# Kernel tuning notes

Hardware: AMD Instinct MI355X
Metric: run time of the kernel (lower is better)

The kernel has to match this reference:

```python
import jax, jax.numpy as jnp
import numpy as np

N, E, D, EDGE_DIM = 50000, 150000, 100, 200

def _w(key, fi, fo):
    return jax.random.normal(key, (fi, fo), dtype=jnp.float32) / np.float32(np.sqrt(fi))

def setup_inputs():
    key = jax.random.key(0)
    ks = jax.random.split(key, 40)
    inp = {}
    inp["x"] = jax.random.normal(ks[0], (N, D), dtype=jnp.float32)
    inp["msg"] = jax.random.normal(ks[1], (E, D), dtype=jnp.float32)
    # TimeEncoder: Linear(1, D)
    inp["time_w"] = _w(ks[2], 1, D)
    inp["time_b"] = jnp.zeros((D,), jnp.float32)
    # TransformerConv 1: in=100, heads=8, out=100, concat -> 800
    H1 = 8 * D
    inp["c1_qw"] = _w(ks[3], D, H1); inp["c1_qb"] = jnp.zeros((H1,), jnp.float32)
    inp["c1_kw"] = _w(ks[4], D, H1); inp["c1_kb"] = jnp.zeros((H1,), jnp.float32)
    inp["c1_vw"] = _w(ks[5], D, H1); inp["c1_vb"] = jnp.zeros((H1,), jnp.float32)
    inp["c1_ew"] = _w(ks[6], EDGE_DIM, H1)  # lin_edge has no bias in PyG
    inp["c1_sw"] = _w(ks[7], D, H1); inp["c1_sb"] = jnp.zeros((H1,), jnp.float32)
    # TransformerConv 2: in=800, heads=1, out=100, concat=False
    inp["c2_qw"] = _w(ks[8], H1, D); inp["c2_qb"] = jnp.zeros((D,), jnp.float32)
    inp["c2_kw"] = _w(ks[9], H1, D); inp["c2_kb"] = jnp.zeros((D,), jnp.float32)
    inp["c2_vw"] = _w(ks[10], H1, D); inp["c2_vb"] = jnp.zeros((D,), jnp.float32)
    inp["c2_ew"] = _w(ks[11], EDGE_DIM, D)
    inp["c2_sw"] = _w(ks[12], H1, D); inp["c2_sb"] = jnp.zeros((D,), jnp.float32)
    # LinkPredictor (in_channels=100, out=2)
    inp["lp_src_w"] = _w(ks[13], D, 2 * D); inp["lp_src_b"] = jnp.zeros((2 * D,), jnp.float32)
    inp["lp_dst_w"] = _w(ks[14], D, 2 * D); inp["lp_dst_b"] = jnp.zeros((2 * D,), jnp.float32)
    inp["lp1_w"] = _w(ks[15], 4 * D, 8 * D); inp["lp1_b"] = jnp.zeros((8 * D,), jnp.float32)
    inp["lp2_w"] = _w(ks[16], 8 * D, 2 * D); inp["lp2_b"] = jnp.zeros((2 * D,), jnp.float32)
    inp["lp3_w"] = _w(ks[17], 2 * D, D // 2); inp["lp3_b"] = jnp.zeros((D // 2,), jnp.float32)
    inp["lp4_w"] = _w(ks[18], D // 2, 2); inp["lp4_b"] = jnp.zeros((2,), jnp.float32)
    inp["last_update"] = jax.random.randint(ks[19], (N,), 0, 1000000)
    inp["t"] = jax.random.randint(ks[20], (E,), 0, 1000000)
    inp["edge_index"] = jax.random.randint(ks[21], (2, E), 0, N)
    return inp

def _tconv(x, src, dst, edge_attr, qw, qb, kw, kb, vw, vb, ew, sw, sb, heads, out_ch, concat, n):
    q = (x @ qw + qb).reshape(n, heads, out_ch)
    k = (x @ kw + kb).reshape(n, heads, out_ch)
    v = (x @ vw + vb).reshape(n, heads, out_ch)
    e = (edge_attr @ ew).reshape(-1, heads, out_ch)        # [E,H,C]
    kj = k[src] + e                                        # gather src keys + edge
    alpha = jnp.sum(q[dst] * kj, axis=-1) / np.float32(np.sqrt(out_ch))  # [E,H]
    amax = jax.ops.segment_max(alpha, dst, num_segments=n)
    ex = jnp.exp(alpha - amax[dst])
    denom = jax.ops.segment_sum(ex, dst, num_segments=n)
    a = ex / (denom[dst] + 1e-16)                          # per-dest softmax
    agg = jax.ops.segment_sum((v[src] + e) * a[..., None], dst, num_segments=n)
    out = agg.reshape(n, heads * out_ch) if concat else jnp.mean(agg, axis=1)
    return out + x @ sw + sb                               # root/skip connection

def reference(x, msg, time_w, time_b,
              c1_qw, c1_qb, c1_kw, c1_kb, c1_vw, c1_vb, c1_ew, c1_sw, c1_sb,
              c2_qw, c2_qb, c2_kw, c2_kb, c2_vw, c2_vb, c2_ew, c2_sw, c2_sb,
              lp_src_w, lp_src_b, lp_dst_w, lp_dst_b,
              lp1_w, lp1_b, lp2_w, lp2_b, lp3_w, lp3_b, lp4_w, lp4_b,
              last_update, t, edge_index):
    src, dst = edge_index[0], edge_index[1]
    rel_t = (last_update[src] - t).astype(jnp.float32)[:, None]  # [E,1]
    rel_enc = jnp.cos(rel_t @ time_w + time_b)                   # [E,D]
    edge_attr = jnp.concatenate([rel_enc, msg], axis=-1)         # [E,200]
    h = jax.nn.relu(_tconv(x, src, dst, edge_attr, c1_qw, c1_qb, c1_kw, c1_kb,
                           c1_vw, c1_vb, c1_ew, c1_sw, c1_sb, 8, D, True, N))
    h = jax.nn.relu(_tconv(h, src, dst, edge_attr, c2_qw, c2_qb, c2_kw, c2_kb,
                           c2_vw, c2_vb, c2_ew, c2_sw, c2_sb, 1, D, False, N))
    hh = jnp.concatenate([h[src] @ lp_src_w + lp_src_b,
                          h[dst] @ lp_dst_w + lp_dst_b], axis=-1)
    hh = jnp.tanh(hh @ lp1_w + lp1_b)
    hh = jnp.tanh(hh @ lp2_w + lp2_b)
    hh = jnp.tanh(hh @ lp3_w + lp3_b)
    return hh @ lp4_w + lp4_b
```

## Files before the change

kernel.cpp:

```cpp
#include <hip/hip_runtime.h>
#include <hip/hip_bf16.h>
#include <math.h>

typedef __hip_bfloat16 bf16;
typedef short s16x8 __attribute__((ext_vector_type(8)));
typedef float f32x4 __attribute__((ext_vector_type(4)));

#define NN 50000
#define EE 150000
#define EH 75000

static __device__ __forceinline__ float b2f(bf16 x){ return __bfloat162float(x); }
static __device__ __forceinline__ bf16 f2b(float x){ return __float2bfloat16(x); }
static __device__ __forceinline__ short f2s(float x){
  union { bf16 b; short s; } u; u.b = f2b(x); return u.s;
}
static __device__ __forceinline__ float u2f_lo(unsigned u){ union{unsigned i;float f;}c; c.i=u<<16; return c.f; }
static __device__ __forceinline__ float u2f_hi(unsigned u){ union{unsigned i;float f;}c; c.i=u&0xffff0000u; return c.f; }

static __device__ __forceinline__ float fast_tanh(float x){
  float a = fabsf(x);
  float e = __expf(2.0f*a);
  float t = 1.0f - __fdividef(2.0f, e + 1.0f);
  return x < 0.f ? -t : t;
}

static __device__ __forceinline__ void gload_lds16(const void* g, void* l){
  __builtin_amdgcn_global_load_lds((const __attribute__((address_space(1))) void*)g,
                                   (__attribute__((address_space(3))) void*)l, 16, 0, 0);
}

template<int N> static __device__ __forceinline__ void wait_vmcnt(){
  if constexpr(N==0) asm volatile("s_waitcnt vmcnt(0)" ::: "memory");
  else if constexpr(N==1) asm volatile("s_waitcnt vmcnt(1)" ::: "memory");
  else if constexpr(N==2) asm volatile("s_waitcnt vmcnt(2)" ::: "memory");
  else if constexpr(N==3) asm volatile("s_waitcnt vmcnt(3)" ::: "memory");
  else if constexpr(N==4) asm volatile("s_waitcnt vmcnt(4)" ::: "memory");
  else if constexpr(N==5) asm volatile("s_waitcnt vmcnt(5)" ::: "memory");
  else asm volatile("s_waitcnt vmcnt(6)" ::: "memory");
}
static __device__ __forceinline__ void wait_lgkm0(){
  asm volatile("s_waitcnt lgkmcnt(0)" ::: "memory");
}
static __device__ __forceinline__ void memfence(){
  asm volatile("" ::: "memory");
}

__global__ void k_zero(int* __restrict__ p, int n){
  int i = blockIdx.x*blockDim.x + threadIdx.x;
  if(i<n) p[i]=0;
}

__global__ void k_hist(const int* __restrict__ dst, int* __restrict__ deg){
  int i = blockIdx.x*blockDim.x + threadIdx.x;
  if(i<EE) atomicAdd(&deg[dst[i]], 1);
}

__global__ void k_scan(const int* __restrict__ deg, int* __restrict__ rowptr){
  __shared__ int part[1024];
  int tid = threadIdx.x;
  const int n = NN;
  int chunk = (n + 1023)/1024;
  int start = tid*chunk;
  int end = start + chunk; if(end > n) end = n;
  int s = 0;
  for(int i=start;i<end;i++) s += deg[i];
  part[tid] = s; __syncthreads();
  for(int off=1; off<1024; off<<=1){
    int v = (tid>=off)? part[tid-off] : 0;
    __syncthreads();
    part[tid] += v;
    __syncthreads();
  }
  int run = (tid==0)? 0 : part[tid-1];
  for(int i=start;i<end;i++){ rowptr[i]=run; run += deg[i]; }
  if(tid==0) rowptr[n] = part[1023];
}

__global__ void k_scatter(const int* __restrict__ dst, const int* __restrict__ srcv,
                          const int* __restrict__ rowptr,
                          int* __restrict__ cursor, int* __restrict__ elist,
                          int* __restrict__ ssrc){
  int e = blockIdx.x*blockDim.x + threadIdx.x;
  if(e<EE){
    int d=dst[e]; int p=atomicAdd(&cursor[d],1);
    int pos = rowptr[d]+p;
    elist[pos]=e; ssrc[pos]=srcv[e];
  }
}

__global__ void k_relenc(const int* __restrict__ elist, const int* __restrict__ ssrc,
                         const int* __restrict__ tt, const int* __restrict__ lu,
                         const float* __restrict__ tw, const float* __restrict__ tb,
                         bf16* __restrict__ rel){
  int i = blockIdx.x*blockDim.x + threadIdx.x;
  if(i >= EE*112) return;
  int j = i/112, c = i - j*112;
  float v = 0.f;
  if(c < 100){
    int e = elist[j];
    float rt  = (float)(lu[ssrc[j]] - tt[e]);
    float arg = __fadd_rn(__fmul_rn(rt, tw[c]), tb[c]);
    v = cosf(arg);
  }
  rel[i] = f2b(v);
}

__global__ void k_cvtpad(const float* __restrict__ in, int incols,
                         bf16* __restrict__ outp, int outcols, int total){
  int i = blockIdx.x*blockDim.x + threadIdx.x;
  if(i >= total) return;
  int r = i/outcols, c = i - r*outcols;
  outp[i] = f2b(c < incols ? in[(size_t)r*incols + c] : 0.f);
}

__global__ void k_wt2(const float* __restrict__ W, int K, int N, int colofs, int ncols,
                      bf16* __restrict__ WT, int kpad, int nrows){
  int i = blockIdx.x*blockDim.x + threadIdx.x;
  if(i >= nrows*kpad) return;
  int n = i / kpad, k = i - n*kpad;
  float v = (n<ncols && k<K)? W[(size_t)k*N + colofs + n] : 0.f;
  WT[i] = f2b(v);
}

__global__ void k_wtc1(const float* __restrict__ qw, const float* __restrict__ kw,
                       const float* __restrict__ vw, bf16* __restrict__ outp){
  int i = blockIdx.x*blockDim.x + threadIdx.x;
  if(i >= 8*320*128) return;
  int h = i/(320*128), r = (i/128)%320, k = i&127;
  float v = 0.f;
  if(r < 300 && k < 100){
    int s = r/100, n = r - s*100;
    const float* W = s==0? qw : s==1? kw : vw;
    v = W[(size_t)k*800 + h*100 + n];
  }
  outp[i] = f2b(v);
}

__global__ void k_wte(const float* __restrict__ ew, int N, int colofs,
                      bf16* __restrict__ outp){
  int i = blockIdx.x*blockDim.x + threadIdx.x;
  if(i >= 112*256) return;
  int r = i>>8, k = i&255;
  float v = 0.f;
  if(r < 100){
    if(k < 100) v = ew[(size_t)k*N + colofs + r];
    else if(k >= 128 && k < 228) v = ew[(size_t)(k-28)*N + colofs + r];
  }
  outp[i] = f2b(v);
}

__global__ void k_bstack3(const float* __restrict__ b0, const float* __restrict__ b1,
                          const float* __restrict__ b2, int W, int H,
                          float* __restrict__ outp){
  int i = blockIdx.x*blockDim.x + threadIdx.x;
  if(i >= H*3*W) return;
  int h = i/(3*W), r = i - h*3*W, s = r/W, c = r - s*W;
  const float* b = s==0? b0 : s==1? b1 : b2;
  outp[i] = b[h*W + c];
}

__global__ void k_foldw(const float* __restrict__ sw, const float* __restrict__ dw,
                        const float* __restrict__ w1, bf16* __restrict__ o){
  int i = blockIdx.x*blockDim.x + threadIdx.x;
  if(i >= 800*224) return;
  int n = i/224, k = i - n*224;
  float s = 0.f;
  if(k < 100){
    for(int j=0;j<200;j++) s += sw[k*200+j]*w1[(size_t)j*800+n];
  } else if(k >= 112 && k < 212){
    int kk = k-112;
    for(int j=0;j<200;j++) s += dw[kk*200+j]*w1[(size_t)(200+j)*800+n];
  }
  o[i] = f2b(s);
}
__global__ void k_foldb(const float* __restrict__ sb, const float* __restrict__ db,
                        const float* __restrict__ w1, const float* __restrict__ b1,
                        float* __restrict__ o){
  int n = blockIdx.x*blockDim.x + threadIdx.x;
  if(n >= 800) return;
  float s = b1[n];
  for(int j=0;j<200;j++) s += sb[j]*w1[(size_t)j*800+n] + db[j]*w1[(size_t)(200+j)*800+n];
  o[n] = s;
}

template<int NT>
static __device__ void mm_body(
    char* lds, int bx, int nstrip,
    const bf16* __restrict__ A1, int lda1, int kv1, const int* __restrict__ g1,
    int KS,
    const bf16* __restrict__ A2b, int lda2b, int kv2b, const int* __restrict__ g2,
    const float* __restrict__ A2f, int lda2f, int kv2f,
    const bf16* __restrict__ WT, int kpad,
    const bf16* __restrict__ zbuf,
    const float* __restrict__ bias,
    bf16* __restrict__ C, int ldc,
    int M, int nvalid, int act)
{
  constexpr int BN = NT*16;
  constexpr int BPASS = (BN*4 + 255)/256;
  constexpr int ABYTES = 8192;
  constexpr int BUFSZ = ABYTES + BPASS*4096;

  const int tid  = threadIdx.x;
  const int wave = tid>>6, lane = tid&63;
  const int quad = lane>>4, lo = lane&15;
  WT += (size_t)nstrip*BN*kpad;
  C  += (size_t)nstrip*BN;
  if(bias) bias += nstrip*BN;
  const int nval = nvalid - nstrip*BN;
  const int row0 = bx*128;

  float bvr[NT];
#pragma unroll
  for(int n=0;n<NT;n++){
    int col = n*16 + lo;
    bvr[n] = (bias && col < nval) ? bias[col] : 0.f;
  }
#pragma unroll
  for(int n=0;n<NT;n++) asm volatile("" :: "v"(bvr[n]));

  const char*  a1b[2];
  const char*  a2bp[2];
  const float* f2base[2];
  int acol0[2];
#pragma unroll
  for(int p=0;p<2;p++){
    int s = p*256 + tid;
    int row = s>>2, cp = s&3;
    int q = cp ^ ((row>>1)&3);
    int col0 = q*8;
    int rg = row0 + row; if(rg > M-1) rg = M-1;
    int r1 = g1 ? g1[rg] : rg;
    int r2 = g2 ? g2[rg] : rg;
    acol0[p] = col0;
    a1b[p]   = (const char*)A1 + ((size_t)r1*lda1 + col0)*2;
    a2bp[p]  = A2b ? (const char*)A2b + ((size_t)r2*lda2b)*2 : nullptr;
    f2base[p]= A2f ? (A2f + (size_t)r2*lda2f) : nullptr;
  }
  const char* bbase[BPASS];
#pragma unroll
  for(int p=0;p<BPASS;p++){
    int s = p*256 + tid;
    int rb = s>>2; if(rb > BN-1) rb = BN-1;
    int cp = s&3;
    int lq = cp ^ ((rb>>1)&3);
    bbase[p] = (const char*)WT + ((size_t)rb*kpad + lq*8)*2;
  }

  f32x4 acc[2][NT];
#pragma unroll
  for(int m=0;m<2;m++)
#pragma unroll
    for(int n=0;n<NT;n++) acc[m][n] = (f32x4){0.f,0.f,0.f,0.f};

  float4 pf0[2], pf1[2];

  auto stageA1 = [&](char* buf, int kb){
#pragma unroll
    for(int p=0;p<2;p++){
      int k = kb + acol0[p];
      const char* s;
      if(k < KS) s = (k < kv1) ? (a1b[p] + (size_t)kb*2) : (const char*)zbuf;
      else { int o = k - KS; s = (o < kv2b) ? (a2bp[p] + (size_t)o*2) : (const char*)zbuf; }
      gload_lds16(s, buf + p*4096 + wave*1024);
    }
  };
  auto loadA2f = [&](int kb){
#pragma unroll
    for(int p=0;p<2;p++){
      int o = kb + acol0[p] - KS;
      const float* ap = f2base[p] + o;
      pf0[p] = (o   < kv2f) ? *(const float4*)ap     : (float4){0.f,0.f,0.f,0.f};
      pf1[p] = (o+4 < kv2f) ? *(const float4*)(ap+4) : (float4){0.f,0.f,0.f,0.f};
    }
  };
  auto writeA2 = [&](char* buf){
#pragma unroll
    for(int p=0;p<2;p++){
      s16x8 v;
      v[0]=f2s(pf0[p].x); v[1]=f2s(pf0[p].y); v[2]=f2s(pf0[p].z); v[3]=f2s(pf0[p].w);
      v[4]=f2s(pf1[p].x); v[5]=f2s(pf1[p].y); v[6]=f2s(pf1[p].z); v[7]=f2s(pf1[p].w);
      *(s16x8*)(buf + p*4096 + (size_t)tid*16) = v;
    }
  };
  auto stageB = [&](char* buf, int kb){
#pragma unroll
    for(int p=0;p<BPASS;p++)
      gload_lds16(bbase[p] + (size_t)kb*2, buf + ABYTES + p*4096 + wave*1024);
  };
  auto compute = [&](const char* buf){
    s16x8 af[2];
#pragma unroll
    for(int m=0;m<2;m++){
      int rl = wave*32 + m*16 + lo;
      int cp = quad ^ ((rl>>1)&3);
      af[m] = *(const s16x8*)(buf + rl*64 + cp*16);
    }
#pragma unroll
    for(int n=0;n<NT;n++){
      int rb = n*16 + lo;
      int cp = quad ^ ((rb>>1)&3);
      s16x8 bfr = *(const s16x8*)(buf + ABYTES + rb*64 + cp*16);
      acc[0][n] = __builtin_amdgcn_mfma_f32_16x16x32_bf16(af[0], bfr, acc[0][n], 0,0,0);
      acc[1][n] = __builtin_amdgcn_mfma_f32_16x16x32_bf16(af[1], bfr, acc[1][n], 0,0,0);
    }
  };

  const int T = kpad >> 5;
  stageA1(lds, 0); stageB(lds, 0);
  if(T > 1){ stageA1(lds + BUFSZ, 32); stageB(lds + BUFSZ, 32); }

  for(int t=0; t<T; t++){
    bool nb  = (t+1 < T);
    bool nfp = nb && A2f && (((t+1)<<5) >= KS);
    if(!nb)      wait_vmcnt<0>();
    else if(nfp) wait_vmcnt<BPASS>();
    else         wait_vmcnt<2+BPASS>();
    wait_lgkm0();
    __builtin_amdgcn_s_barrier();
    memfence();
    int tp = t+2;
    bool sp  = (tp < T);
    bool spf = sp && A2f && ((tp<<5) >= KS);
    char* nb3 = lds + (tp%3)*BUFSZ;
    if(sp){
      int kb2 = tp<<5;
      if(spf) loadA2f(kb2);
      else    stageA1(nb3, kb2);
      stageB(nb3, kb2);
    }
    compute(lds + (t%3)*BUFSZ);
    if(spf) writeA2(nb3);
  }

  const int r0 = (lane&1)<<1;
#pragma unroll
  for(int n=0;n<NT;n++){
    int col  = n*16 + lo;
    int pcol = col & ~1;
    bool cok = (pcol < nval);
    float bv = bvr[n];
#pragma unroll
    for(int m=0;m<2;m++){
      float v[4];
#pragma unroll
      for(int r=0;r<4;r++){
        float t = acc[m][n][r] + bv;
        if(act==1) t = fmaxf(t, 0.f);
        else if(act==2) t = fast_tanh(t);
        v[r] = t;
      }
      unsigned mylo = (unsigned)(unsigned short)f2s(v[r0])
                    | ((unsigned)(unsigned short)f2s(v[r0+1])<<16);
      unsigned snd  = (unsigned)(unsigned short)f2s(v[r0^2])
                    | ((unsigned)(unsigned short)f2s(v[(r0^2)+1])<<16);
      unsigned got  = (unsigned)__shfl_xor((int)snd, 1);
      unsigned w0, w1;
      if(lane&1){ w0 = (got & 0xffffu) | (mylo<<16); w1 = (got>>16) | (mylo & 0xffff0000u); }
      else      { w0 = (mylo & 0xffffu) | (got<<16); w1 = (mylo>>16) | (got & 0xffff0000u); }
      if(cok){
        int prow = row0 + wave*32 + m*16 + quad*4 + r0;
        if(prow   < M) *(unsigned*)(C + (size_t)prow*ldc + pcol) = w0;
        if(prow+1 < M) *(unsigned*)(C + (size_t)(prow+1)*ldc + pcol) = w1;
      }
    }
  }
}

template<int NT>
__global__ __launch_bounds__(256) void mm_tile(
    const bf16* A1, int lda1, int kv1, const int* g1, int KS,
    const bf16* A2b, int lda2b, int kv2b, const int* g2,
    const float* A2f, int lda2f, int kv2f,
    const bf16* WT, int kpad, const bf16* zbuf, const float* bias,
    bf16* C, int ldc, int M, int nvalid, int act)
{
  constexpr int BUFSZ = 8192 + ((NT*16*4+255)/256)*4096;
  __shared__ __align__(16) char lds[3*BUFSZ];
  mm_body<NT>(lds, blockIdx.x, blockIdx.y, A1,lda1,kv1,g1, KS,
              A2b,lda2b,kv2b,g2, A2f,lda2f,kv2f, WT,kpad, zbuf, bias,
              C,ldc, M,nvalid,act);
}

template<int NT>
__global__ __launch_bounds__(256) void mm_gath(
    const bf16* __restrict__ A, int lda, int KS,
    const int* __restrict__ gs, const int* __restrict__ gd,
    const bf16* __restrict__ WT,
    const float* __restrict__ bias,
    bf16* __restrict__ C, int ldc,
    int M, int nvalid, int act)
{
  constexpr int T = 7;
  constexpr int KPAD = 224;
  constexpr int BN = NT*16;
  constexpr int BPASS = (BN*4 + 255)/256;
  constexpr int BUFSZ = BPASS*4096;
  __shared__ __align__(16) char lds[3*BUFSZ];

  const int tid  = threadIdx.x;
  const int wave = tid>>6, lane = tid&63;
  const int quad = lane>>4, lo = lane&15;
  const int nstrip = blockIdx.y;
  const bf16* WTs = WT + (size_t)nstrip*BN*KPAD;
  C += (size_t)nstrip*BN;
  const float* bp = bias ? bias + nstrip*BN : nullptr;
  const int nval = nvalid - nstrip*BN;
  const int row0 = blockIdx.x*128;

  float bvr[NT];
#pragma unroll
  for(int n=0;n<NT;n++){
    int col = n*16 + lo;
    bvr[n] = (bp && col < nval) ? bp[col] : 0.f;
  }

  const bf16* abase[2][2];
#pragma unroll
  for(int m=0;m<2;m++){
    int r = row0 + wave*32 + m*16 + lo; if(r > M-1) r = M-1;
    abase[m][0] = A + (size_t)gs[r]*lda;
    abase[m][1] = A + (size_t)gd[r]*lda;
  }

  s16x8 areg[T][2];
#pragma unroll
  for(int t=0;t<T;t++){
#pragma unroll
    for(int m=0;m<2;m++){
      int k = t*32 + quad*8;
      const bf16* p = (k < KS) ? (abase[m][0] + k) : (abase[m][1] + (k - KS));
      asm volatile("global_load_dwordx4 %0, %1, off"
                   : "=v"(areg[t][m]) : "v"(p));
    }
  }
  memfence();

  const char* bbase[BPASS];
#pragma unroll
  for(int p=0;p<BPASS;p++){
    int s = p*256 + tid;
    int rb = s>>2; if(rb > BN-1) rb = BN-1;
    int cp = s&3;
    int lq = cp ^ ((rb>>1)&3);
    bbase[p] = (const char*)WTs + ((size_t)rb*KPAD + lq*8)*2;
  }
  auto stageB = [&](char* buf, int kb){
#pragma unroll
    for(int p=0;p<BPASS;p++)
      gload_lds16(bbase[p] + (size_t)kb*2, buf + p*4096 + wave*1024);
  };

  f32x4 acc[2][NT];
#pragma unroll
  for(int m=0;m<2;m++)
#pragma unroll
    for(int n=0;n<NT;n++) acc[m][n] = (f32x4){0.f,0.f,0.f,0.f};

  stageB(lds, 0);
  stageB(lds + BUFSZ, 32);

#pragma unroll
  for(int t=0; t<T; t++){
    if(t < T-1) wait_vmcnt<BPASS>();
    else        wait_vmcnt<0>();
    wait_lgkm0();
    __builtin_amdgcn_s_barrier();
    memfence();
    if(t+2 < T) stageB(lds + ((t+2)%3)*BUFSZ, (t+2)*32);
    const char* buf = lds + (t%3)*BUFSZ;
#pragma unroll
    for(int n=0;n<NT;n++){
      int rb = n*16 + lo;
      int cp = quad ^ ((rb>>1)&3);
      s16x8 bfr = *(const s16x8*)(buf + rb*64 + cp*16);
      acc[0][n] = __builtin_amdgcn_mfma_f32_16x16x32_bf16(areg[t][0], bfr, acc[0][n], 0,0,0);
      acc[1][n] = __builtin_amdgcn_mfma_f32_16x16x32_bf16(areg[t][1], bfr, acc[1][n], 0,0,0);
    }
  }

  const int r0 = (lane&1)<<1;
#pragma unroll
  for(int n=0;n<NT;n++){
    int col  = n*16 + lo;
    int pcol = col & ~1;
    bool cok = (pcol < nval);
    float bv = bvr[n];
#pragma unroll
    for(int m=0;m<2;m++){
      float v[4];
#pragma unroll
      for(int r=0;r<4;r++){
        float t = acc[m][n][r] + bv;
        if(act==1) t = fmaxf(t, 0.f);
        else if(act==2) t = fast_tanh(t);
        v[r] = t;
      }
      unsigned mylo = (unsigned)(unsigned short)f2s(v[r0])
                    | ((unsigned)(unsigned short)f2s(v[r0+1])<<16);
      unsigned snd  = (unsigned)(unsigned short)f2s(v[r0^2])
                    | ((unsigned)(unsigned short)f2s(v[(r0^2)+1])<<16);
      unsigned got  = (unsigned)__shfl_xor((int)snd, 1);
      unsigned w0, w1;
      if(lane&1){ w0 = (got & 0xffffu) | (mylo<<16); w1 = (got>>16) | (mylo & 0xffff0000u); }
      else      { w0 = (mylo & 0xffffu) | (got<<16); w1 = (mylo>>16) | (got & 0xffff0000u); }
      if(cok){
        int prow = row0 + wave*32 + m*16 + quad*4 + r0;
        if(prow   < M) *(unsigned*)(C + (size_t)prow*ldc + pcol) = w0;
        if(prow+1 < M) *(unsigned*)(C + (size_t)(prow+1)*ldc + pcol) = w1;
      }
    }
  }
}

__global__ __launch_bounds__(256) void k_attn(
    const int* __restrict__ rowptr, const int* __restrict__ ssrc,
    const bf16* __restrict__ qkv, const bf16* __restrict__ ehc,
    bf16* __restrict__ hout, int ldh, int colofs, int zpad)
{
  int wave = threadIdx.x>>6, lane = threadIdx.x&63;
  int node = blockIdx.x*4 + wave;
  if(node >= NN) return;
  bool act = (lane < 50);
  float q0=0.f, q1=0.f;
  const unsigned* qrow = (const unsigned*)(qkv + (size_t)node*300);
  if(act){ unsigned u = qrow[lane]; q0=u2f_lo(u); q1=u2f_hi(u); }
  int s0 = rowptr[node], s1 = rowptr[node+1];
  float m = -3.4e38f, d = 0.f, a0 = 0.f, a1 = 0.f;
  for(int j=s0; j<s1; j++){
    int sn = ssrc[j];
    float p = 0.f, e0=0.f, e1=0.f;
    if(act){
      unsigned uk = ((const unsigned*)(qkv + (size_t)sn*300 + 100))[lane];
      unsigned ue = ((const unsigned*)(ehc + (size_t)j*100))[lane];
      e0=u2f_lo(ue); e1=u2f_hi(ue);
      p = q0*(u2f_lo(uk)+e0) + q1*(u2f_hi(uk)+e1);
    }
    for(int off=32; off; off>>=1) p += __shfl_xor(p, off);
    float alpha = p * 0.1f;
    float mn = fmaxf(m, alpha);
    float sc = __expf(m - mn);
    float wv = __expf(alpha - mn);
    d = d*sc + wv;
    if(act){
      unsigned uv = ((const unsigned*)(qkv + (size_t)sn*300 + 200))[lane];
      a0 = a0*sc + wv*(u2f_lo(uv)+e0);
      a1 = a1*sc + wv*(u2f_hi(uv)+e1);
    }
    m = mn;
  }
  if(act){
    float inv = 1.f/(d + 1e-16f);
    unsigned us = ((const unsigned*)(hout + (size_t)node*ldh + colofs))[lane];
    float h0 = fmaxf(u2f_lo(us) + a0*inv, 0.f);
    float h1 = fmaxf(u2f_hi(us) + a1*inv, 0.f);
    bf16* op = hout + (size_t)node*ldh + colofs + lane*2;
    op[0] = f2b(h0); op[1] = f2b(h1);
  } else if(zpad && lane < 56){
    bf16* op = hout + (size_t)node*ldh + colofs + lane*2;
    op[0] = f2b(0.f); op[1] = f2b(0.f);
  }
}

__global__ void k_lpout(const bf16* __restrict__ t3, const float* __restrict__ w4,
                        const float* __restrict__ b4, float* __restrict__ out,
                        int base, int n){
  int i = blockIdx.x*blockDim.x + threadIdx.x;
  if(i >= n*2) return;
  int g = i>>1, j = i&1;
  const bf16* tp = t3 + (size_t)g*50;
  float s = 0.f;
  for(int k=0;k<50;k++) s += b2f(tp[k])*w4[k*2+j];
  out[(size_t)(base+g)*2 + j] = s + b4[j];
}

extern "C" void kernel_launch(void* const* d_in, const int* in_sizes, int n_in,
                              void* d_out, int out_size, void* d_ws, size_t ws_size,
                              hipStream_t stream){
  const float* x       = (const float*)d_in[0];
  const float* msg     = (const float*)d_in[1];
  const float* time_w  = (const float*)d_in[2];
  const float* time_b  = (const float*)d_in[3];
  const float* c1_qw=(const float*)d_in[4];  const float* c1_qb=(const float*)d_in[5];
  const float* c1_kw=(const float*)d_in[6];  const float* c1_kb=(const float*)d_in[7];
  const float* c1_vw=(const float*)d_in[8];  const float* c1_vb=(const float*)d_in[9];
  const float* c1_ew=(const float*)d_in[10];
  const float* c1_sw=(const float*)d_in[11]; const float* c1_sb=(const float*)d_in[12];
  const float* c2_qw=(const float*)d_in[13]; const float* c2_qb=(const float*)d_in[14];
  const float* c2_kw=(const float*)d_in[15]; const float* c2_kb=(const float*)d_in[16];
  const float* c2_vw=(const float*)d_in[17]; const float* c2_vb=(const float*)d_in[18];
  const float* c2_ew=(const float*)d_in[19];
  const float* c2_sw=(const float*)d_in[20]; const float* c2_sb=(const float*)d_in[21];
  const float* lp_src_w=(const float*)d_in[22]; const float* lp_src_b=(const float*)d_in[23];
  const float* lp_dst_w=(const float*)d_in[24]; const float* lp_dst_b=(const float*)d_in[25];
  const float* lp1_w=(const float*)d_in[26]; const float* lp1_b=(const float*)d_in[27];
  const float* lp2_w=(const float*)d_in[28]; const float* lp2_b=(const float*)d_in[29];
  const float* lp3_w=(const float*)d_in[30]; const float* lp3_b=(const float*)d_in[31];
  const float* lp4_w=(const float*)d_in[32]; const float* lp4_b=(const float*)d_in[33];
  const int* last_update=(const int*)d_in[34];
  const int* tt =(const int*)d_in[35];
  const int* edge_index=(const int*)d_in[36];
  const int* src = edge_index;
  const int* dst = edge_index + EE;
  float* out = (float*)d_out;

  char* ws = (char*)d_ws;
  bf16*  h1    = (bf16*) (ws + 0);
  bf16*  relc  = (bf16*) (ws + 80000000);
  bf16*  ehc   = (bf16*) (ws + 113600000);
  bf16*  qkv   = (bf16*) (ws + 143600000);
  bf16*  h2p   = (bf16*) (ws + 183600000);
  bf16*  xb    = (bf16*) (ws + 183600000);
  int*   rowptr= (int*)  (ws + 194800000);
  int*   elist = (int*)  (ws + 195000064);
  int*   ssrc  = (int*)  (ws + 195600064);
  int*   deg   = (int*)  (ws + 196200064);
  int*   cursor= (int*)  (ws + 196400064);
  bf16* c1all  = (bf16*)(ws + 196600064);
  bf16* c1eall = (bf16*)(ws + 197255424);
  bf16* c1swt  = (bf16*)(ws + 197714176);
  bf16* c2all  = (bf16*)(ws + 197918976);
  bf16* c2swt  = (bf16*)(ws + 198430976);
  bf16* c2e    = (bf16*)(ws + 198610176);
  bf16* lp1tF  = (bf16*)(ws + 198667520);
  bf16* lp2t   = (bf16*)(ws + 199025920);
  bf16* lp3t   = (bf16*)(ws + 199384320);
  float* c1ball= (float*)(ws + 199412992);
  float* c2ball= (float*)(ws + 199422592);
  float* lp1c  = (float*)(ws + 199423808);
  bf16* zbuf   = (bf16*)(ws + 199427008);
  bf16* lt1 = (bf16*)(ws + 0);
  bf16* lt2 = (bf16*)(ws + 120000000);
  bf16* lt3 = (bf16*)(ws + 150000000);

  k_wtc1<<<(8*320*128+255)/256,256,0,stream>>>(c1_qw,c1_kw,c1_vw,c1all);
  for(int h=0; h<8; h++)
    k_wte<<<(112*256+255)/256,256,0,stream>>>(c1_ew, 800, h*100, c1eall + (size_t)h*112*256);
  k_wte<<<(112*256+255)/256,256,0,stream>>>(c2_ew, 100, 0, c2e);
  k_wt2<<<(800*128+255)/256,256,0,stream>>>(c1_sw,100,800,0,800,c1swt,128,800);
  k_wt2<<<(100*800+255)/256,256,0,stream>>>(c2_qw,800,100,0,100,c2all,         800,100);
  k_wt2<<<(100*800+255)/256,256,0,stream>>>(c2_kw,800,100,0,100,c2all+100*800, 800,100);
  k_wt2<<<(100*800+255)/256,256,0,stream>>>(c2_vw,800,100,0,100,c2all+200*800, 800,100);
  k_wt2<<<(20*800+255)/256,256,0,stream>>>(c2_qw,800,100,0,0,   c2all+300*800, 800,20);
  k_wt2<<<(112*800+255)/256,256,0,stream>>>(c2_sw,800,100,0,100,c2swt,800,112);
  k_wt2<<<(224*800+255)/256,256,0,stream>>>(lp2_w,800,200,0,200,lp2t,800,224);
  k_wt2<<<(64*224+255)/256,256,0,stream>>>(lp3_w,200,50,0,50,lp3t,224,64);
  k_foldw<<<(800*224+255)/256,256,0,stream>>>(lp_src_w, lp_dst_w, lp1_w, lp1tF);
  k_foldb<<<(800+255)/256,256,0,stream>>>(lp_src_b, lp_dst_b, lp1_w, lp1_b, lp1c);
  k_bstack3<<<(8*300+255)/256,256,0,stream>>>(c1_qb,c1_kb,c1_vb,100,8,c1ball);
  k_bstack3<<<(300+255)/256,256,0,stream>>>(c2_qb,c2_kb,c2_vb,100,1,c2ball);
  k_zero<<<1,64,0,stream>>>((int*)zbuf, 16);
  k_cvtpad<<<(NN*112+255)/256,256,0,stream>>>(x, 100, xb, 112, NN*112);

  k_zero   <<<(NN+255)/256, 256, 0, stream>>>(deg, NN);
  k_zero   <<<(NN+255)/256, 256, 0, stream>>>(cursor, NN);
  k_hist   <<<(EE+255)/256, 256, 0, stream>>>(dst, deg);
  k_scan   <<<1, 1024, 0, stream>>>(deg, rowptr);
  k_scatter<<<(EE+255)/256, 256, 0, stream>>>(dst, src, rowptr, cursor, elist, ssrc);

  k_relenc<<<(EE*112+255)/256, 256, 0, stream>>>(elist, ssrc, tt, last_update,
                                                 time_w, time_b, relc);

  int gN = (NN + 127)/128;
  int gE = (EE + 127)/128;
  int gL = (EH + 127)/128;
  int gA = (NN + 3)/4;

  mm_tile<10><<<dim3(gN,5),256,0,stream>>>(xb,112,112,nullptr, 128,
      nullptr,0,0,nullptr, nullptr,0,0,
      c1swt,128, zbuf, c1_sb, h1,800, NN,800,0);

  for(int h=0; h<8; h++){
    mm_tile<10><<<dim3(gN,2),256,0,stream>>>(xb,112,112,nullptr, 128,
        nullptr,0,0,nullptr, nullptr,0,0,
        c1all + (size_t)h*320*128, 128, zbuf, c1ball + h*300, qkv,300, NN,300,0);
    mm_tile<7><<<dim3(gE,1),256,0,stream>>>(relc,112,112,nullptr, 128,
        nullptr,0,0,elist, msg,100,100,
        c1eall + (size_t)h*112*256, 256, zbuf, nullptr, ehc,100, EE,100,0);
    k_attn<<<gA,256,0,stream>>>(rowptr, ssrc, qkv, ehc, h1, 800, h*100, 0);
  }

  mm_tile<10><<<dim3(gN,2),256,0,stream>>>(h1,800,800,nullptr, 800,
      nullptr,0,0,nullptr, nullptr,0,0,
      c2all,800, zbuf, c2ball, qkv,300, NN,300,0);
  mm_tile<7><<<dim3(gE,1),256,0,stream>>>(relc,112,112,nullptr, 128,
      nullptr,0,0,elist, msg,100,100,
      c2e,256, zbuf, nullptr, ehc,100, EE,100,0);
  mm_tile<7><<<dim3(gN,1),256,0,stream>>>(h1,800,800,nullptr, 800,
      nullptr,0,0,nullptr, nullptr,0,0,
      c2swt,800, zbuf, c2_sb, h2p,112, NN,100,0);
  k_attn<<<gA,256,0,stream>>>(rowptr, ssrc, qkv, ehc, h2p, 112, 0, 1);

  for(int half=0; half<2; half++){
    const int* esrc = src + half*EH;
    const int* edst = dst + half*EH;
    mm_gath<10><<<dim3(gL,5),256,0,stream>>>(h2p,112,112, esrc, edst,
        lp1tF, lp1c, lt1,800, EH,800,2);
    mm_tile<7><<<dim3(gL,2),256,0,stream>>>(lt1,800,800,nullptr, 800,
        nullptr,0,0,nullptr, nullptr,0,0,
        lp2t,800, zbuf, lp2_b, lt2,200, EH,200,2);
    mm_tile<4><<<dim3(gL,1),256,0,stream>>>(lt2,200,200,nullptr, 224,
        nullptr,0,0,nullptr, nullptr,0,0,
        lp3t,224, zbuf, lp3_b, lt3,50, EH,50,2);
    k_lpout<<<(EH*2+255)/256,256,0,stream>>>(lt3, lp4_w, lp4_b, out, half*EH, EH);
  }

  (void)in_sizes; (void)n_in; (void)out_size; (void)ws_size;
}
```

Baseline: 1.972 ms.

## Merge per-layer node and edge GEMM launches into one multi-task kernel

Adds a k_cv kernel that dispatches on block index to run the node QKV projection, the edge projection, and optionally the skip projection in a single launch. This replaces three separate mm_tile launches per head and per layer, using NT=10 for all of them, with edge and skip weights padded to 160 rows. The weight transposes for the eight heads are batched into one launch, and the two zeroing kernels are merged into one. The aim is to cut launch overhead and tail idle time by letting independent GEMMs fill the GPU together. In exchange, the edge and skip GEMMs now compute wider padded tiles than before.

```diff
diff --git a/kernel.cpp b/kernel.cpp
--- a/kernel.cpp
+++ b/kernel.cpp
@@ -9,6 +9,8 @@
 #define NN 50000
 #define EE 150000
 #define EH 75000
+#define GN 391
+#define GE 1172
 
 static __device__ __forceinline__ float b2f(bf16 x){ return __bfloat162float(x); }
 static __device__ __forceinline__ bf16 f2b(float x){ return __float2bfloat16(x); }
@@ -137,11 +139,12 @@
   outp[i] = f2b(v);
 }
 
-__global__ void k_wte(const float* __restrict__ ew, int N, int colofs,
+__global__ void k_wte(const float* __restrict__ ew, int N, int H,
                       bf16* __restrict__ outp){
   int i = blockIdx.x*blockDim.x + threadIdx.x;
-  if(i >= 112*256) return;
-  int r = i>>8, k = i&255;
+  if(i >= H*160*256) return;
+  int h = i/(160*256), r = (i/256)%160, k = i&255;
+  int colofs = h*100;
   float v = 0.f;
   if(r < 100){
     if(k < 100) v = ew[(size_t)k*N + colofs + r];
@@ -381,6 +384,42 @@
   mm_body<NT>(lds, blockIdx.x, blockIdx.y, A1,lda1,kv1,g1, KS,
               A2b,lda2b,kv2b,g2, A2f,lda2f,kv2f, WT,kpad, zbuf, bias,
               C,ldc, M,nvalid,act);
+}
+
+__global__ __launch_bounds__(256) void k_cv(
+    int n0, const bf16* A0, int lda0, int kpad0, const bf16* W0,
+    const float* b0, bf16* C0, int ldc0, int nv0,
+    int n1, const bf16* Ae, const float* msg, const int* elist, const bf16* We,
+    bf16* Ce,
+    int n2, const bf16* A2, int lda2, int kpad2, const bf16* W2,
+    const float* b2, bf16* C2, int ldc2, int nv2,
+    const bf16* zbuf)
+{
+  __shared__ __align__(16) char lds[3*20480];
+  int bx = blockIdx.x;
+  const bf16* A1; int lda1, kv1, KS;
+  const float* A2f = nullptr; int lda2f = 0, kv2f = 0; const int* g2 = nullptr;
+  const bf16* WT; int kpad; const float* bias; bf16* C; int ldc, M, nval;
+  int brow, strip;
+  if(bx < n0){
+    strip = bx >= GN ? 1 : 0; brow = bx - strip*GN;
+    A1 = A0; lda1 = lda0; kv1 = lda0; KS = kpad0;
+    WT = W0; kpad = kpad0; bias = b0; C = C0; ldc = ldc0; M = NN; nval = nv0;
+  } else if(bx < n0 + n1){
+    brow = bx - n0; strip = 0;
+    A1 = Ae; lda1 = 112; kv1 = 112; KS = 128;
+    A2f = msg; lda2f = 100; kv2f = 100; g2 = elist;
+    WT = We; kpad = 256; bias = nullptr; C = Ce; ldc = 100; M = EE; nval = 100;
+  } else {
+    int t = bx - n0 - n1; strip = 0;
+    while(t >= GN){ t -= GN; strip++; }
+    brow = t;
+    A1 = A2; lda1 = lda2; kv1 = lda2; KS = kpad2;
+    WT = W2; kpad = kpad2; bias = b2; C = C2; ldc = ldc2; M = NN; nval = nv2;
+  }
+  mm_body<10>(lds, brow, strip, A1, lda1, kv1, nullptr, KS,
+              nullptr, 0, 0, g2, A2f, lda2f, kv2f,
+              WT, kpad, zbuf, bias, C, ldc, M, nval, 0);
 }
 
 template<int NT>
@@ -619,31 +658,30 @@
   int*   cursor= (int*)  (ws + 196400064);
   bf16* c1all  = (bf16*)(ws + 196600064);
   bf16* c1eall = (bf16*)(ws + 197255424);
-  bf16* c1swt  = (bf16*)(ws + 197714176);
-  bf16* c2all  = (bf16*)(ws + 197918976);
-  bf16* c2swt  = (bf16*)(ws + 198430976);
-  bf16* c2e    = (bf16*)(ws + 198610176);
-  bf16* lp1tF  = (bf16*)(ws + 198667520);
-  bf16* lp2t   = (bf16*)(ws + 199025920);
-  bf16* lp3t   = (bf16*)(ws + 199384320);
-  float* c1ball= (float*)(ws + 199412992);
-  float* c2ball= (float*)(ws + 199422592);
-  float* lp1c  = (float*)(ws + 199423808);
-  bf16* zbuf   = (bf16*)(ws + 199427008);
+  bf16* c1swt  = (bf16*)(ws + 197910784);
+  bf16* c2all  = (bf16*)(ws + 198115584);
+  bf16* c2swt  = (bf16*)(ws + 198627584);
+  bf16* c2e    = (bf16*)(ws + 198883584);
+  bf16* lp1tF  = (bf16*)(ws + 198965504);
+  bf16* lp2t   = (bf16*)(ws + 199323904);
+  bf16* lp3t   = (bf16*)(ws + 199682304);
+  float* c1ball= (float*)(ws + 199710976);
+  float* c2ball= (float*)(ws + 199720576);
+  float* lp1c  = (float*)(ws + 199721792);
+  bf16* zbuf   = (bf16*)(ws + 199725056);
   bf16* lt1 = (bf16*)(ws + 0);
   bf16* lt2 = (bf16*)(ws + 120000000);
   bf16* lt3 = (bf16*)(ws + 150000000);
 
   k_wtc1<<<(8*320*128+255)/256,256,0,stream>>>(c1_qw,c1_kw,c1_vw,c1all);
-  for(int h=0; h<8; h++)
-    k_wte<<<(112*256+255)/256,256,0,stream>>>(c1_ew, 800, h*100, c1eall + (size_t)h*112*256);
-  k_wte<<<(112*256+255)/256,256,0,stream>>>(c2_ew, 100, 0, c2e);
+  k_wte<<<(8*160*256+255)/256,256,0,stream>>>(c1_ew, 800, 8, c1eall);
+  k_wte<<<(160*256+255)/256,256,0,stream>>>(c2_ew, 100, 1, c2e);
   k_wt2<<<(800*128+255)/256,256,0,stream>>>(c1_sw,100,800,0,800,c1swt,128,800);
   k_wt2<<<(100*800+255)/256,256,0,stream>>>(c2_qw,800,100,0,100,c2all,         800,100);
   k_wt2<<<(100*800+255)/256,256,0,stream>>>(c2_kw,800,100,0,100,c2all+100*800, 800,100);
   k_wt2<<<(100*800+255)/256,256,0,stream>>>(c2_vw,800,100,0,100,c2all+200*800, 800,100);
   k_wt2<<<(20*800+255)/256,256,0,stream>>>(c2_qw,800,100,0,0,   c2all+300*800, 800,20);
-  k_wt2<<<(112*800+255)/256,256,0,stream>>>(c2_sw,800,100,0,100,c2swt,800,112);
+  k_wt2<<<(160*800+255)/256,256,0,stream>>>(c2_sw,800,100,0,100,c2swt,800,160);
   k_wt2<<<(224*800+255)/256,256,0,stream>>>(lp2_w,800,200,0,200,lp2t,800,224);
   k_wt2<<<(64*224+255)/256,256,0,stream>>>(lp3_w,200,50,0,50,lp3t,224,64);
   k_foldw<<<(800*224+255)/256,256,0,stream>>>(lp_src_w, lp_dst_w, lp1_w, lp1tF);
@@ -653,8 +691,7 @@
   k_zero<<<1,64,0,stream>>>((int*)zbuf, 16);
   k_cvtpad<<<(NN*112+255)/256,256,0,stream>>>(x, 100, xb, 112, NN*112);
 
-  k_zero   <<<(NN+255)/256, 256, 0, stream>>>(deg, NN);
-  k_zero   <<<(NN+255)/256, 256, 0, stream>>>(cursor, NN);
+  k_zero   <<<(2*NN+255)/256, 256, 0, stream>>>(deg, 2*NN);
   k_hist   <<<(EE+255)/256, 256, 0, stream>>>(dst, deg);
   k_scan   <<<1, 1024, 0, stream>>>(deg, rowptr);
   k_scatter<<<(EE+255)/256, 256, 0, stream>>>(dst, src, rowptr, cursor, elist, ssrc);
@@ -662,34 +699,24 @@
   k_relenc<<<(EE*112+255)/256, 256, 0, stream>>>(elist, ssrc, tt, last_update,
                                                  time_w, time_b, relc);
 
-  int gN = (NN + 127)/128;
-  int gE = (EE + 127)/128;
   int gL = (EH + 127)/128;
   int gA = (NN + 3)/4;
 
-  mm_tile<10><<<dim3(gN,5),256,0,stream>>>(xb,112,112,nullptr, 128,
-      nullptr,0,0,nullptr, nullptr,0,0,
-      c1swt,128, zbuf, c1_sb, h1,800, NN,800,0);
-
   for(int h=0; h<8; h++){
-    mm_tile<10><<<dim3(gN,2),256,0,stream>>>(xb,112,112,nullptr, 128,
-        nullptr,0,0,nullptr, nullptr,0,0,
-        c1all + (size_t)h*320*128, 128, zbuf, c1ball + h*300, qkv,300, NN,300,0);
-    mm_tile<7><<<dim3(gE,1),256,0,stream>>>(relc,112,112,nullptr, 128,
-        nullptr,0,0,elist, msg,100,100,
-        c1eall + (size_t)h*112*256, 256, zbuf, nullptr, ehc,100, EE,100,0);
+    int n2 = (h==0) ? 5*GN : 0;
+    k_cv<<<2*GN + GE + n2, 256, 0, stream>>>(
+        2*GN, xb, 112, 128, c1all + (size_t)h*320*128, c1ball + h*300, qkv, 300, 300,
+        GE, relc, msg, elist, c1eall + (size_t)h*160*256, ehc,
+        n2, xb, 112, 128, c1swt, c1_sb, h1, 800, 800,
+        zbuf);
     k_attn<<<gA,256,0,stream>>>(rowptr, ssrc, qkv, ehc, h1, 800, h*100, 0);
   }
 
-  mm_tile<10><<<dim3(gN,2),256,0,stream>>>(h1,800,800,nullptr, 800,
-      nullptr,0,0,nullptr, nullptr,0,0,
-      c2all,800, zbuf, c2ball, qkv,300, NN,300,0);
-  mm_tile<7><<<dim3(gE,1),256,0,stream>>>(relc,112,112,nullptr, 128,
-      nullptr,0,0,elist, msg,100,100,
-      c2e,256, zbuf, nullptr, ehc,100, EE,100,0);
-  mm_tile<7><<<dim3(gN,1),256,0,stream>>>(h1,800,800,nullptr, 800,
-      nullptr,0,0,nullptr, nullptr,0,0,
-      c2swt,800, zbuf, c2_sb, h2p,112, NN,100,0);
+  k_cv<<<2*GN + GE + GN, 256, 0, stream>>>(
+      2*GN, h1, 800, 800, c2all, c2ball, qkv, 300, 300,
+      GE, relc, msg, elist, c2e, ehc,
+      GN, h1, 800, 800, c2swt, c2_sb, h2p, 112, 100,
+      zbuf);
   k_attn<<<gA,256,0,stream>>>(rowptr, ssrc, qkv, ehc, h2p, 112, 0, 1);
 
   for(int half=0; half<2; half++){
```

After: 1.967 ms. About the same (-0.3%).
